# Performance work log

Hardware: AMD Instinct MI355X
Metric: run time of the kernel (lower is better)

## Reference

```python
import jax, jax.numpy as jnp
import numpy as np

C = 128      # hidden_dim
H = 8        # nheads
HD = C // H  # head_dim = 16
SCALE = HD ** (-0.5)
Q = 100      # num_queries
T = 5        # t
DM = 512     # d_model
AD = 128     # audio feature dim
EPS = 1e-5


def _ln(x, g, b):
    m = jnp.mean(x, -1, keepdims=True)
    v = jnp.mean((x - m) ** 2, -1, keepdims=True)
    return (x - m) / jnp.sqrt(v + EPS) * g + b


def _heads(x):
    bt, L, c = x.shape
    return x.reshape(bt, L, H, c // H).transpose(0, 2, 1, 3)  # (bt,H,L,hd)


def _unheads(x):
    bt, h, L, d = x.shape
    return x.transpose(0, 2, 1, 3).reshape(bt, L, h * d)


def _attn(q, k, v):
    a = jax.nn.softmax(jnp.einsum('bhqd,bhkd->bhqk', q, k) * SCALE, axis=-1)
    return jnp.einsum('bhqk,bhkd->bhqd', a, v)


def setup_inputs() -> dict:
    key = jax.random.key(0)
    ks = iter(jax.random.split(key, 40))
    def nrm(shape, s=0.02):
        return jax.random.normal(next(ks), shape, dtype=jnp.float32) * s
    bt, hw = 40, 1024
    return {
        'audio_feat': jax.random.normal(next(ks), (bt, hw, AD), dtype=jnp.float32),
        'vis_feat': jax.random.normal(next(ks), (bt, hw, DM), dtype=jnp.float32),
        'iq_emb': nrm((Q, C), 0.1),
        'w_iqp': nrm((C, 2 * C)), 'b_iqp': jnp.zeros((2 * C,), jnp.float32),
        'w_afp': nrm((AD, 2 * C)), 'b_afp': jnp.zeros((2 * C,), jnp.float32),
        'w_vfp': nrm((DM, 2 * C)), 'b_vfp': jnp.zeros((2 * C,), jnp.float32),
        'g_an': jnp.ones((2 * C,), jnp.float32), 'be_an': jnp.zeros((2 * C,), jnp.float32),
        'g_vn': jnp.ones((2 * C,), jnp.float32), 'be_vn': jnp.zeros((2 * C,), jnp.float32),
        'w_aqp': nrm((C, 2 * C)), 'b_aqp': jnp.zeros((2 * C,), jnp.float32),
        'w_vqp': nrm((C, 2 * C)), 'b_vqp': jnp.zeros((2 * C,), jnp.float32),
        'w_aq': nrm((AD, C)), 'b_aq': jnp.zeros((C,), jnp.float32),
        'w_vq': nrm((DM, C)), 'b_vq': jnp.zeros((C,), jnp.float32),
        'w_in': nrm((C, 3 * C)), 'b_in': jnp.zeros((3 * C,), jnp.float32),
        'w_o': nrm((C, C)), 'b_o': jnp.zeros((C,), jnp.float32),
        'w_ao': nrm((C, DM)), 'b_ao': jnp.zeros((DM,), jnp.float32),
        'w_vo': nrm((C, DM)), 'b_vo': jnp.zeros((DM,), jnp.float32),
    }


def reference(audio_feat, vis_feat, iq_emb, w_iqp, b_iqp, w_afp, b_afp,
              w_vfp, b_vfp, g_an, be_an, g_vn, be_vn, w_aqp, b_aqp,
              w_vqp, b_vqp, w_aq, b_aq, w_vq, b_vq, w_in, b_in, w_o, b_o,
              w_ao, b_ao, w_vo, b_vo):
    bt, hw, _ = vis_feat.shape
    bs = bt // T

    # intermediate query projection -> audio / vis query sets
    aq0, vq0 = jnp.split(iq_emb @ w_iqp + b_iqp, 2, axis=-1)  # (Q, C) each
    aqh = _heads(jnp.broadcast_to(aq0, (bt, Q, C)))
    vqh = _heads(jnp.broadcast_to(vq0, (bt, Q, C)))

    # feature K/V (LayerNorm over 2C then chunk)
    a_ki, a_vi = jnp.split(_ln(audio_feat @ w_afp + b_afp, g_an, be_an), 2, axis=-1)
    v_ki, v_vi = jnp.split(_ln(vis_feat @ w_vfp + b_vfp, g_vn, be_vn), 2, axis=-1)

    # cross-attn: queries attend to features, with residual on queries
    aiq = _unheads(_attn(aqh, _heads(a_ki), _heads(a_vi)) + aqh)  # (bt,Q,C)
    viq = _unheads(_attn(vqh, _heads(v_ki), _heads(v_vi)) + vqh)

    # self-attn over concatenated queries across time (per sample)
    queries = jnp.concatenate([aiq, viq], axis=1).reshape(bs, T * 2 * Q, C)
    qkv = queries @ w_in + b_in
    q, k, v = jnp.split(qkv, 3, axis=-1)
    sa = _unheads(_attn(_heads(q), _heads(k), _heads(v))) @ w_o + b_o
    queries = sa.reshape(bt, 2 * Q, C)
    aiq2, viq2 = queries[:, :Q], queries[:, Q:]

    # fused queries become K/V for the features
    a_kf, a_vf = jnp.split(aiq2 @ w_aqp + b_aqp, 2, axis=-1)
    v_kf, v_vf = jnp.split(viq2 @ w_vqp + b_vqp, 2, axis=-1)
    _a = _heads(audio_feat @ w_aq + b_aq)
    _v = _heads(vis_feat @ w_vq + b_vq)

    a_att = _unheads(_attn(_a, _heads(v_kf), _heads(v_vf)))  # (bt,hw,C)
    audio_out = (a_att + audio_feat) @ w_ao + b_ao            # (bt,hw,DM)

    v_att = _unheads(_attn(_v, _heads(a_kf), _heads(a_vf)))   # (bt,hw,C)
    vis_out = v_att @ w_vo + b_vo + vis_feat                  # (bt,hw,DM)

    return (audio_out, vis_out, aiq2)
```

## Files before the change

### kernel.cpp

```cpp
#include <hip/hip_runtime.h>

#define EPSF 1e-5f
#define SCALEF 0.25f

typedef __attribute__((ext_vector_type(8))) __bf16 bf16x8;
typedef __attribute__((ext_vector_type(8))) unsigned short sh8;
typedef __attribute__((ext_vector_type(4))) float f32x4;

__device__ __forceinline__ unsigned short f2bf(float f) {
  return __builtin_bit_cast(unsigned short, (__bf16)f);
}
__device__ __forceinline__ unsigned pk2(float lo, float hi) {
  return (unsigned)f2bf(lo) | ((unsigned)f2bf(hi) << 16);
}
__device__ __forceinline__ float bf2f(unsigned short u) {
  return __uint_as_float((unsigned)u << 16);
}

__device__ __forceinline__ void gll16(const void* g, void* l) {
  __builtin_amdgcn_global_load_lds((const __attribute__((address_space(1))) void*)g,
                                   (__attribute__((address_space(3))) void*)l,
                                   16, 0, 0);
}

template <int K, int BN, int EPI, bool POST, bool AHEAD, bool OBF, bool PBF, bool QSC>
__global__ __launch_bounds__(BN * 2) void mfma_gemm(
    const unsigned short* __restrict__ A, const unsigned short* __restrict__ Wt,
    const float* __restrict__ bias, const float* __restrict__ post,
    float* __restrict__ C, int M, int Ntot, int ATPB, int CTPB, size_t CPS,
    float* __restrict__ aiq2) {
  constexpr int NW = BN / 32;
  constexpr int NCW = BN / 64;
  __shared__ __align__(16) unsigned short As[128 * 32];
  __shared__ __align__(16) unsigned short Bs[BN * 32];
  const int tid = threadIdx.x;
  const int wid = tid >> 6, lane = tid & 63;
  const int wr = wid / NCW, wc = wid % NCW;
  const int m0t = blockIdx.x * 128, n0t = blockIdx.y * BN;
  const int ir = lane >> 2, sl = lane & 3;
  const int sg = lane >> 4, li = lane & 15;
  f32x4 acc[4][4];
#pragma unroll
  for (int i = 0; i < 4; i++)
#pragma unroll
    for (int j = 0; j < 4; j++) acc[i][j] = (f32x4){0.f, 0.f, 0.f, 0.f};
  constexpr int nIss = 8 + BN / 16;

  for (int k0 = 0; k0 < K; k0 += 32) {
    __syncthreads();
    for (int is = wid; is < nIss; is += NW) {
      if (is < 8) {
        int r = is * 16 + ir;
        int sp = sl ^ ((r >> 1) & 3);
        const unsigned short* gsrc;
        if (AHEAD) {
          int rg = m0t + r;
          if (rg >= M) rg = M - 1;
          int b = rg / ATPB, tok = rg - b * ATPB;
          int e = k0 + sp * 8;
          gsrc = A + ((((size_t)b * 8 + (e >> 4)) * ATPB + tok) << 4) + (e & 15);
        } else {
          gsrc = A + (size_t)(m0t + r) * K + k0 + sp * 8;
        }
        gll16(gsrc, (void*)&As[is * 512]);
      } else {
        int r = (is - 8) * 16 + ir;
        int sp = sl ^ ((r >> 1) & 3);
        gll16(Wt + (size_t)(n0t + r) * K + k0 + sp * 8, (void*)&Bs[(is - 8) * 512]);
      }
    }
    __syncthreads();
    bf16x8 af[4], bfr[4];
#pragma unroll
    for (int mi = 0; mi < 4; mi++) {
      int m = wr * 64 + mi * 16 + li;
      sh8 t = *(const sh8*)&As[m * 32 + ((sg ^ ((m >> 1) & 3)) << 3)];
      af[mi] = __builtin_bit_cast(bf16x8, t);
    }
#pragma unroll
    for (int ni = 0; ni < 4; ni++) {
      int n = wc * 64 + ni * 16 + li;
      sh8 t = *(const sh8*)&Bs[n * 32 + ((sg ^ ((n >> 1) & 3)) << 3)];
      bfr[ni] = __builtin_bit_cast(bf16x8, t);
    }
#pragma unroll
    for (int mi = 0; mi < 4; mi++)
#pragma unroll
      for (int ni = 0; ni < 4; ni++)
        acc[mi][ni] = __builtin_amdgcn_mfma_f32_16x16x32_bf16(af[mi], bfr[ni],
                                                              acc[mi][ni], 0, 0, 0);
  }

  float bv[4];
#pragma unroll
  for (int ni = 0; ni < 4; ni++) bv[ni] = bias[n0t + wc * 64 + ni * 16 + li];

  if constexpr (EPI == 2) {
#pragma unroll
    for (int mi = 0; mi < 4; mi++)
#pragma unroll
      for (int r = 0; r < 4; r++) {
        int mg = m0t + wr * 64 + mi * 16 + sg * 4 + r;
        if (mg < M) {
          int b = mg / CTPB, tok = mg - b * CTPB;
#pragma unroll
          for (int ni = 0; ni < 4; ni++) {
            int col = n0t + wc * 64 + ni * 16 + li;
            float v = acc[mi][ni][r] + bv[ni];
            int pt = col >> 7, h = (col >> 4) & 7, d = col & 15;
            if (QSC && pt == 0) v *= SCALEF;
            size_t idx = ((((size_t)b * 8 + h) * CTPB + tok) << 4) + d;
            if (OBF)
              ((unsigned short*)C + (size_t)pt * CPS)[idx] = f2bf(v);
            else
              (C + (size_t)pt * CPS)[idx] = v;
          }
        }
      }
  } else {
#pragma unroll
    for (int mi = 0; mi < 4; mi++)
#pragma unroll
      for (int r = 0; r < 4; r++) {
        int mrow = m0t + wr * 64 + mi * 16 + sg * 4 + r;
        if (mrow < M) {
#pragma unroll
          for (int ni = 0; ni < 4; ni++) {
            int col = n0t + wc * 64 + ni * 16 + li;
            float v = acc[mi][ni][r] + bv[ni];
            if (POST) {
              if (PBF)
                v += bf2f(((const unsigned short*)post)[(size_t)mrow * Ntot + col]);
              else
                v += post[(size_t)mrow * Ntot + col];
            }
            C[(size_t)mrow * Ntot + col] = v;
            if (aiq2) {
              int fb = mrow / 200, wi2 = mrow % 200;
              if (wi2 < 100) aiq2[((size_t)fb * 100 + wi2) * Ntot + col] = v;
            }
          }
        }
      }
  }
}

__global__ __launch_bounds__(512) void ln_gemm(
    const float* __restrict__ audio, const float* __restrict__ vis,
    const unsigned short* __restrict__ afp_t, const unsigned short* __restrict__ vfp_t,
    const float* __restrict__ b_afp, const float* __restrict__ b_vfp,
    const float* __restrict__ g_an, const float* __restrict__ g_vn,
    const float* __restrict__ be_an, const float* __restrict__ be_vn,
    unsigned short* __restrict__ akn, unsigned short* __restrict__ vkn,
    unsigned short* __restrict__ audio_bf, unsigned short* __restrict__ vis_bf) {
  constexpr int BN = 256, NW = 8, NCW = 4;
  constexpr size_t CPS = 5242880;
  __shared__ __align__(16) unsigned short As[128 * 32];
  __shared__ __align__(16) unsigned short Bs[BN * 32];
  __shared__ float2 part[128][4];
  const int z = blockIdx.z;
  const float* Af32 = z ? vis : audio;
  const unsigned short* Wt = z ? vfp_t : afp_t;
  const float* bias = z ? b_vfp : b_afp;
  const float* gg = z ? g_vn : g_an;
  const float* be = z ? be_vn : be_an;
  unsigned short* C = z ? vkn : akn;
  unsigned short* Aside = z ? vis_bf : audio_bf;
  const int K = z ? 512 : 128;
  const int tid = threadIdx.x;
  const int wid = tid >> 6, lane = tid & 63;
  const int wr = wid / NCW, wc = wid % NCW;
  const int m0t = blockIdx.x * 128;
  const int ir = lane >> 2, sl = lane & 3;
  const int sg = lane >> 4, li = lane & 15;
  f32x4 acc[4][4];
#pragma unroll
  for (int i = 0; i < 4; i++)
#pragma unroll
    for (int j = 0; j < 4; j++) acc[i][j] = (f32x4){0.f, 0.f, 0.f, 0.f};

  for (int k0 = 0; k0 < K; k0 += 32) {
    __syncthreads();
    {
      int r = tid >> 2, slp = tid & 3;
      int sp = slp ^ ((r >> 1) & 3);
      const float4* src = (const float4*)(Af32 + (size_t)(m0t + r) * K + k0 + sp * 8);
      float4 aa = src[0], bb = src[1];
      uint4 w;
      w.x = pk2(aa.x, aa.y); w.y = pk2(aa.z, aa.w);
      w.z = pk2(bb.x, bb.y); w.w = pk2(bb.z, bb.w);
      *(uint4*)&As[r * 32 + slp * 8] = w;
      *(uint4*)(Aside + (size_t)(m0t + r) * K + k0 + sp * 8) = w;
    }
    for (int is = 8 + wid; is < 8 + BN / 16; is += NW) {
      int r2 = (is - 8) * 16 + ir;
      int sp2 = sl ^ ((r2 >> 1) & 3);
      gll16(Wt + (size_t)r2 * K + k0 + sp2 * 8, (void*)&Bs[(is - 8) * 512]);
    }
    __syncthreads();
    bf16x8 af[4], bfr[4];
#pragma unroll
    for (int mi = 0; mi < 4; mi++) {
      int m = wr * 64 + mi * 16 + li;
      sh8 t = *(const sh8*)&As[m * 32 + ((sg ^ ((m >> 1) & 3)) << 3)];
      af[mi] = __builtin_bit_cast(bf16x8, t);
    }
#pragma unroll
    for (int ni = 0; ni < 4; ni++) {
      int n = wc * 64 + ni * 16 + li;
      sh8 t = *(const sh8*)&Bs[n * 32 + ((sg ^ ((n >> 1) & 3)) << 3)];
      bfr[ni] = __builtin_bit_cast(bf16x8, t);
    }
#pragma unroll
    for (int mi = 0; mi < 4; mi++)
#pragma unroll
      for (int ni = 0; ni < 4; ni++)
        acc[mi][ni] = __builtin_amdgcn_mfma_f32_16x16x32_bf16(af[mi], bfr[ni],
                                                              acc[mi][ni], 0, 0, 0);
  }

  float bv[4];
#pragma unroll
  for (int ni = 0; ni < 4; ni++) bv[ni] = bias[wc * 64 + ni * 16 + li];
#pragma unroll
  for (int mi = 0; mi < 4; mi++)
#pragma unroll
    for (int ni = 0; ni < 4; ni++)
#pragma unroll
      for (int r = 0; r < 4; r++) acc[mi][ni][r] += bv[ni];
#pragma unroll
  for (int mi = 0; mi < 4; mi++)
#pragma unroll
    for (int r = 0; r < 4; r++) {
      float s = acc[mi][0][r] + acc[mi][1][r] + acc[mi][2][r] + acc[mi][3][r];
      float q2 = acc[mi][0][r] * acc[mi][0][r] + acc[mi][1][r] * acc[mi][1][r] +
                 acc[mi][2][r] * acc[mi][2][r] + acc[mi][3][r] * acc[mi][3][r];
#pragma unroll
      for (int off = 1; off < 16; off <<= 1) {
        s += __shfl_xor(s, off);
        q2 += __shfl_xor(q2, off);
      }
      if (li == 0) part[wr * 64 + mi * 16 + sg * 4 + r][wc] = make_float2(s, q2);
    }
  __syncthreads();
  float gv[4], bev[4];
#pragma unroll
  for (int ni = 0; ni < 4; ni++) {
    int col = wc * 64 + ni * 16 + li;
    gv[ni] = gg[col];
    bev[ni] = be[col];
  }
#pragma unroll
  for (int mi = 0; mi < 4; mi++)
#pragma unroll
    for (int r = 0; r < 4; r++) {
      int mrow = wr * 64 + mi * 16 + sg * 4 + r;
      float2 p0 = part[mrow][0], p1 = part[mrow][1], p2 = part[mrow][2], p3 = part[mrow][3];
      float S = p0.x + p1.x + p2.x + p3.x;
      float Qq = p0.y + p1.y + p2.y + p3.y;
      float mean = S * (1.f / 256.f);
      float var = Qq * (1.f / 256.f) - mean * mean;
      float rstd = rsqrtf(var + EPSF);
      int mg = m0t + mrow;
      int b = mg >> 10, tok = mg & 1023;
#pragma unroll
      for (int ni = 0; ni < 4; ni++) {
        int col = wc * 64 + ni * 16 + li;
        float val = (acc[mi][ni][r] - mean) * rstd * gv[ni] + bev[ni];
        int half = col >> 7, h = (col >> 4) & 7, d = col & 15;
        size_t idx = ((((size_t)b * 8 + h) * 1024 + tok) << 4) + d;
        (C + (half ? CPS : 0))[idx] = f2bf(val);
      }
    }
}

__global__ __launch_bounds__(256) void projq_kernel(
    const unsigned short* __restrict__ audio_bf, const unsigned short* __restrict__ vis_bf,
    const unsigned short* __restrict__ aq_t, const unsigned short* __restrict__ vq_t,
    const float* __restrict__ b_aq, const float* __restrict__ b_vq,
    unsigned short* __restrict__ a_hm, unsigned short* __restrict__ v_hm) {
  constexpr int BN = 128, NW = 4, NCW = 2;
  __shared__ __align__(16) unsigned short As[128 * 32];
  __shared__ __align__(16) unsigned short Bs[BN * 32];
  const int z = blockIdx.z;
  const unsigned short* A = z ? vis_bf : audio_bf;
  const unsigned short* Wt = z ? vq_t : aq_t;
  const float* bias = z ? b_vq : b_aq;
  unsigned short* C = z ? v_hm : a_hm;
  const int K = z ? 512 : 128;
  const int tid = threadIdx.x;
  const int wid = tid >> 6, lane = tid & 63;
  const int wr = wid / NCW, wc = wid % NCW;
  const int m0t = blockIdx.x * 128;
  const int ir = lane >> 2, sl = lane & 3;
  const int sg = lane >> 4, li = lane & 15;
  f32x4 acc[4][4];
#pragma unroll
  for (int i = 0; i < 4; i++)
#pragma unroll
    for (int j = 0; j < 4; j++) acc[i][j] = (f32x4){0.f, 0.f, 0.f, 0.f};

  for (int k0 = 0; k0 < K; k0 += 32) {
    __syncthreads();
    for (int is = wid; is < 8 + BN / 16; is += NW) {
      if (is < 8) {
        int r = is * 16 + ir;
        int sp = sl ^ ((r >> 1) & 3);
        gll16(A + (size_t)(m0t + r) * K + k0 + sp * 8, (void*)&As[is * 512]);
      } else {
        int r = (is - 8) * 16 + ir;
        int sp = sl ^ ((r >> 1) & 3);
        gll16(Wt + (size_t)r * K + k0 + sp * 8, (void*)&Bs[(is - 8) * 512]);
      }
    }
    __syncthreads();
    bf16x8 af[4], bfr[4];
#pragma unroll
    for (int mi = 0; mi < 4; mi++) {
      int m = wr * 64 + mi * 16 + li;
      sh8 t = *(const sh8*)&As[m * 32 + ((sg ^ ((m >> 1) & 3)) << 3)];
      af[mi] = __builtin_bit_cast(bf16x8, t);
    }
#pragma unroll
    for (int ni = 0; ni < 4; ni++) {
      int n = wc * 64 + ni * 16 + li;
      sh8 t = *(const sh8*)&Bs[n * 32 + ((sg ^ ((n >> 1) & 3)) << 3)];
      bfr[ni] = __builtin_bit_cast(bf16x8, t);
    }
#pragma unroll
    for (int mi = 0; mi < 4; mi++)
#pragma unroll
      for (int ni = 0; ni < 4; ni++)
        acc[mi][ni] = __builtin_amdgcn_mfma_f32_16x16x32_bf16(af[mi], bfr[ni],
                                                              acc[mi][ni], 0, 0, 0);
  }

  float bv[4];
#pragma unroll
  for (int ni = 0; ni < 4; ni++) bv[ni] = bias[wc * 64 + ni * 16 + li];
#pragma unroll
  for (int mi = 0; mi < 4; mi++)
#pragma unroll
    for (int r = 0; r < 4; r++) {
      int mg = m0t + wr * 64 + mi * 16 + sg * 4 + r;
      int b = mg >> 10, tok = mg & 1023;
#pragma unroll
      for (int ni = 0; ni < 4; ni++) {
        int col = wc * 64 + ni * 16 + li;
        float v = (acc[mi][ni][r] + bv[ni]) * SCALEF;
        int h = (col >> 4) & 7, d = col & 15;
        C[((((size_t)b * 8 + h) * 1024 + tok) << 4) + d] = f2bf(v);
      }
    }
}

__global__ __launch_bounds__(512) void mattn1(
    const float* __restrict__ aqvq,
    const unsigned short* __restrict__ akn, const unsigned short* __restrict__ avn,
    const unsigned short* __restrict__ vkn, const unsigned short* __restrict__ vvn,
    unsigned short* __restrict__ op) {
  __shared__ __align__(16) unsigned short Klds[64][24];
  __shared__ __align__(16) unsigned short VTlds[16][72];
  __shared__ __align__(16) unsigned short Plds[8][16][72];
  const int tid = threadIdx.x, wid = tid >> 6, lane = tid & 63;
  const int li = lane & 15, gr = lane >> 4;
  const int z = blockIdx.z, h = blockIdx.y;
  const int mod = z >= 40 ? 1 : 0;
  const int b = z - mod * 40;
  const int bh = b * 8 + h;
  const int qi = wid * 16 + li;
  const bool qact = qi < 100;
  const int qic = qact ? qi : 99;
  const float* qrow = aqvq + mod * 128 + (size_t)qic * 256 + h * 16;
  const unsigned short* kp = mod ? vkn : akn;
  const unsigned short* vp = mod ? vvn : avn;

  sh8 z8 = (sh8)0;
  bf16x8 qf = __builtin_bit_cast(bf16x8, z8);
  if (gr < 2) {
    const float4* q4 = (const float4*)(qrow + gr * 8);
    float4 qa = q4[0], qb = q4[1];
    sh8 tt;
    tt[0] = f2bf(qa.x * SCALEF); tt[1] = f2bf(qa.y * SCALEF);
    tt[2] = f2bf(qa.z * SCALEF); tt[3] = f2bf(qa.w * SCALEF);
    tt[4] = f2bf(qb.x * SCALEF); tt[5] = f2bf(qb.y * SCALEF);
    tt[6] = f2bf(qb.z * SCALEF); tt[7] = f2bf(qb.w * SCALEF);
    qf = __builtin_bit_cast(bf16x8, tt);
  }

  float mrun = -3e38f, lrun = 0.f;
  f32x4 acc = (f32x4){0.f, 0.f, 0.f, 0.f};
  const f32x4 zero4 = (f32x4){0.f, 0.f, 0.f, 0.f};
  const unsigned* Ku = (const unsigned*)(kp + (size_t)bh * 1024 * 16);
  const unsigned* Vu = (const unsigned*)(vp + (size_t)bh * 1024 * 16);
  const int skey = tid >> 3, sdb = tid & 7;

  unsigned kw = Ku[(size_t)skey * 8 + sdb];
  unsigned vw = Vu[(size_t)skey * 8 + sdb];
  for (int kb = 0; kb < 1024; kb += 64) {
    __syncthreads();
    *(unsigned*)&Klds[skey][sdb * 2] = kw;
    VTlds[sdb * 2 + 0][skey] = (unsigned short)(vw & 0xffff);
    VTlds[sdb * 2 + 1][skey] = (unsigned short)(vw >> 16);
    if (kb + 64 < 1024) {
      kw = Ku[(size_t)(kb + 64 + skey) * 8 + sdb];
      vw = Vu[(size_t)(kb + 64 + skey) * 8 + sdb];
    }
    __syncthreads();
    f32x4 st[4];
#pragma unroll
    for (int t = 0; t < 4; t++) {
      sh8 kk = *(const sh8*)&Klds[t * 16 + li][(gr & 1) * 8];
      st[t] = __builtin_amdgcn_mfma_f32_16x16x32_bf16(
          __builtin_bit_cast(bf16x8, kk), qf, zero4, 0, 0, 0);
    }
    float bm = st[0][0];
#pragma unroll
    for (int t = 0; t < 4; t++)
#pragma unroll
      for (int r = 0; r < 4; r++) bm = fmaxf(bm, st[t][r]);
    bm = fmaxf(bm, __shfl_xor(bm, 16));
    bm = fmaxf(bm, __shfl_xor(bm, 32));
    if (bm > mrun + 8.f) {
      float cf = __expf(mrun - bm);
      lrun *= cf;
      acc[0] *= cf; acc[1] *= cf; acc[2] *= cf; acc[3] *= cf;
      mrun = bm;
    }
    float ls = 0.f;
    unsigned pw[4][2];
#pragma unroll
    for (int t = 0; t < 4; t++) {
      float p0 = __expf(st[t][0] - mrun), p1 = __expf(st[t][1] - mrun);
      float p2 = __expf(st[t][2] - mrun), p3 = __expf(st[t][3] - mrun);
      ls += (p0 + p1) + (p2 + p3);
      pw[t][0] = pk2(p0, p1);
      pw[t][1] = pk2(p2, p3);
    }
    ls += __shfl_xor(ls, 16);
    ls += __shfl_xor(ls, 32);
    lrun += ls;
#pragma unroll
    for (int t = 0; t < 4; t++)
      *(uint2*)&Plds[wid][li][t * 16 + gr * 4] = make_uint2(pw[t][0], pw[t][1]);
#pragma unroll
    for (int hh = 0; hh < 2; hh++) {
      sh8 vt = *(const sh8*)&VTlds[li][hh * 32 + gr * 8];
      sh8 pt = *(const sh8*)&Plds[wid][li][hh * 32 + gr * 8];
      acc = __builtin_amdgcn_mfma_f32_16x16x32_bf16(
          __builtin_bit_cast(bf16x8, vt), __builtin_bit_cast(bf16x8, pt), acc, 0, 0, 0);
    }
  }
  float inv = 1.f / lrun;
  float o[4];
#pragma unroll
  for (int r = 0; r < 4; r++) o[r] = acc[r] * inv;
  const float4* q4 = (const float4*)(qrow + gr * 4);
  float4 qv = q4[0];
  o[0] += qv.x; o[1] += qv.y; o[2] += qv.z; o[3] += qv.w;
  if (qact) {
    int obh = (b / 5) * 8 + h;
    int otok = (b % 5) * 200 + mod * 100 + qi;
    *(uint2*)(op + (((size_t)obh * 1000 + otok) << 4) + gr * 4) =
        make_uint2(pk2(o[0], o[1]), pk2(o[2], o[3]));
  }
}

template <int MODE>
__global__ __launch_bounds__(512) void mattn8(
    const unsigned short* __restrict__ q0s, const unsigned short* __restrict__ q1s,
    size_t qsb, size_t qsh, int qsr,
    const unsigned short* __restrict__ k0s, const unsigned short* __restrict__ v0s,
    const unsigned short* __restrict__ k1s, const unsigned short* __restrict__ v1s,
    int nk, int nq, unsigned short* __restrict__ o0s, unsigned short* __restrict__ o1s,
    int OTPB, const unsigned short* __restrict__ residbf) {
  __shared__ __align__(16) unsigned short Klds[64][24];
  __shared__ __align__(16) unsigned short VTlds[16][72];
  __shared__ __align__(16) unsigned short Plds[8][16][72];
  const int tid = threadIdx.x, wid = tid >> 6, lane = tid & 63;
  const int li = lane & 15, gr = lane >> 4;
  const int z = blockIdx.z, h = blockIdx.y;
  int mod = 0, b = z;
  const unsigned short *qp = q0s, *kp = k0s, *vp = v0s;
  unsigned short* op = o0s;
  if (MODE == 2) {
    mod = z >= 40 ? 1 : 0;
    b = z - mod * 40;
    if (mod) { qp = q1s; kp = k1s; vp = v1s; op = o1s; }
  }
  const int bh = b * 8 + h;
  const int qi = blockIdx.x * 128 + wid * 16 + li;
  const bool qact = qi < nq;
  const int qic = qact ? qi : nq - 1;
  const unsigned short* qrow = qp + b * qsb + h * qsh + (size_t)qic * qsr;

  sh8 z8 = (sh8)0;
  bf16x8 qf = __builtin_bit_cast(bf16x8, z8);
  if (gr < 2) qf = __builtin_bit_cast(bf16x8, *(const sh8*)(qrow + gr * 8));

  float mrun = -3e38f, lrun = 0.f;
  f32x4 acc = (f32x4){0.f, 0.f, 0.f, 0.f};
  const f32x4 zero4 = (f32x4){0.f, 0.f, 0.f, 0.f};
  const unsigned* Ku = (const unsigned*)(kp + (size_t)bh * nk * 16);
  const unsigned* Vu = (const unsigned*)(vp + (size_t)bh * nk * 16);
  const int skey = tid >> 3, sdb = tid & 7;

  unsigned kw = (skey < nk) ? Ku[(size_t)skey * 8 + sdb] : 0u;
  unsigned vw = (skey < nk) ? Vu[(size_t)skey * 8 + sdb] : 0u;
  for (int kb = 0; kb < nk; kb += 64) {
    __syncthreads();
    *(unsigned*)&Klds[skey][sdb * 2] = kw;
    VTlds[sdb * 2 + 0][skey] = (unsigned short)(vw & 0xffff);
    VTlds[sdb * 2 + 1][skey] = (unsigned short)(vw >> 16);
    if (kb + 64 < nk) {
      int gk = kb + 64 + skey;
      kw = (gk < nk) ? Ku[(size_t)gk * 8 + sdb] : 0u;
      vw = (gk < nk) ? Vu[(size_t)gk * 8 + sdb] : 0u;
    }
    __syncthreads();
    f32x4 st[4];
#pragma unroll
    for (int t = 0; t < 4; t++) {
      sh8 kk = *(const sh8*)&Klds[t * 16 + li][(gr & 1) * 8];
      st[t] = __builtin_amdgcn_mfma_f32_16x16x32_bf16(
          __builtin_bit_cast(bf16x8, kk), qf, zero4, 0, 0, 0);
    }
    if (kb + 64 > nk) {
#pragma unroll
      for (int t = 0; t < 4; t++) {
        int kbase = kb + t * 16 + gr * 4;
#pragma unroll
        for (int r = 0; r < 4; r++)
          if (kbase + r >= nk) st[t][r] = -1e30f;
      }
    }
    float bm = st[0][0];
#pragma unroll
    for (int t = 0; t < 4; t++)
#pragma unroll
      for (int r = 0; r < 4; r++) bm = fmaxf(bm, st[t][r]);
    bm = fmaxf(bm, __shfl_xor(bm, 16));
    bm = fmaxf(bm, __shfl_xor(bm, 32));
    if (bm > mrun + 8.f) {
      float cf = __expf(mrun - bm);
      lrun *= cf;
      acc[0] *= cf; acc[1] *= cf; acc[2] *= cf; acc[3] *= cf;
      mrun = bm;
    }
    float ls = 0.f;
    unsigned pw[4][2];
#pragma unroll
    for (int t = 0; t < 4; t++) {
      float p0 = __expf(st[t][0] - mrun), p1 = __expf(st[t][1] - mrun);
      float p2 = __expf(st[t][2] - mrun), p3 = __expf(st[t][3] - mrun);
      ls += (p0 + p1) + (p2 + p3);
      pw[t][0] = pk2(p0, p1);
      pw[t][1] = pk2(p2, p3);
    }
    ls += __shfl_xor(ls, 16);
    ls += __shfl_xor(ls, 32);
    lrun += ls;
#pragma unroll
    for (int t = 0; t < 4; t++)
      *(uint2*)&Plds[wid][li][t * 16 + gr * 4] = make_uint2(pw[t][0], pw[t][1]);
#pragma unroll
    for (int hh = 0; hh < 2; hh++) {
      sh8 vt = *(const sh8*)&VTlds[li][hh * 32 + gr * 8];
      sh8 pt = *(const sh8*)&Plds[wid][li][hh * 32 + gr * 8];
      acc = __builtin_amdgcn_mfma_f32_16x16x32_bf16(
          __builtin_bit_cast(bf16x8, vt), __builtin_bit_cast(bf16x8, pt), acc, 0, 0, 0);
    }
  }
  float inv = 1.f / lrun;
  float o[4];
#pragma unroll
  for (int r = 0; r < 4; r++) o[r] = acc[r] * inv;
  if (MODE == 2 && mod == 0 && residbf) {
    uint2 rv = *(const uint2*)(residbf + ((size_t)b * 1024 + qic) * 128 + h * 16 + gr * 4);
    o[0] += bf2f((unsigned short)(rv.x & 0xffff));
    o[1] += bf2f((unsigned short)(rv.x >> 16));
    o[2] += bf2f((unsigned short)(rv.y & 0xffff));
    o[3] += bf2f((unsigned short)(rv.y >> 16));
  }
  if (qact) {
    *(uint2*)(op + (((size_t)bh * OTPB + qi) << 4) + gr * 4) =
        make_uint2(pk2(o[0], o[1]), pk2(o[2], o[3]));
  }
}

__global__ __launch_bounds__(256) void prep_kernel(
    const float* __restrict__ iq, const float* __restrict__ w_iqp,
    const float* __restrict__ b_iqp,
    const float* __restrict__ w_afp, const float* __restrict__ w_vfp,
    const float* __restrict__ w_aq, const float* __restrict__ w_vq,
    const float* __restrict__ w_in, const float* __restrict__ w_o,
    const float* __restrict__ w_ao, const float* __restrict__ w_vo,
    unsigned short* __restrict__ WT, float* __restrict__ aqvq) {
  __shared__ float row[128];
  const int g = blockIdx.x, tid = threadIdx.x;
  if (g < 1728) {
    int lg = g;
    int K, N;
    const float* W;
    unsigned dst;
    if (lg < 128)       { K = 128; N = 256; W = w_afp; dst = 0; }
    else if (lg < 640)  { K = 512; N = 256; W = w_vfp; dst = 32768;  lg -= 128; }
    else if (lg < 704)  { K = 128; N = 128; W = w_aq;  dst = 163840; lg -= 640; }
    else if (lg < 960)  { K = 512; N = 128; W = w_vq;  dst = 180224; lg -= 704; }
    else if (lg < 1152) { K = 128; N = 384; W = w_in;  dst = 245760; lg -= 960; }
    else if (lg < 1216) { K = 128; N = 128; W = w_o;   dst = 294912; lg -= 1152; }
    else if (lg < 1472) { K = 128; N = 512; W = w_ao;  dst = 311296; lg -= 1216; }
    else                { K = 128; N = 512; W = w_vo;  dst = 376832; lg -= 1472; }
    int idx = lg * 256 + tid;
    if (idx < K * N) {
      int k = idx / N, n = idx - k * N;
      WT[dst + (size_t)n * K + k] = f2bf(W[idx]);
    }
  } else {
    int r = g - 1728;
    if (tid < 128) row[tid] = iq[r * 128 + tid];
    __syncthreads();
    float acc = b_iqp[tid];
#pragma unroll 8
    for (int k = 0; k < 128; ++k) acc += row[k] * w_iqp[k * 256 + tid];
    aqvq[r * 256 + tid] = acc;
  }
}

template <int K, int N, int R>
__global__ __launch_bounds__(N) void gemm_kv_kernel(
    const float* __restrict__ in,
    const float* __restrict__ Wa, const float* __restrict__ ba,
    const float* __restrict__ Wv, const float* __restrict__ bvv,
    unsigned short* __restrict__ Ka, unsigned short* __restrict__ Va,
    unsigned short* __restrict__ Kv, unsigned short* __restrict__ Vv) {
  __shared__ float rows[R][K];
  const int sel = blockIdx.y;
  const float* W = sel ? Wv : Wa;
  const float* bias = sel ? bvv : ba;
  unsigned short* outK = sel ? Kv : Ka;
  unsigned short* outV = sel ? Vv : Va;
  const int rowoff = sel ? 100 : 0;
  int r0 = blockIdx.x * R;
  for (int e = threadIdx.x; e < R * K; e += N) {
    int rr = e / K, k = e - rr * K;
    size_t r = r0 + rr;
    size_t irx = (r / 100) * 200 + rowoff + (r % 100);
    rows[rr][k] = in[irx * K + k];
  }
  __syncthreads();
  int c = threadIdx.x;
  float acc[R];
  float bb = bias[c];
#pragma unroll
  for (int rr = 0; rr < R; rr++) acc[rr] = bb;
  for (int k = 0; k < K; k += 4) {
    float w0 = W[(size_t)k * N + c];
    float w1 = W[(size_t)(k + 1) * N + c];
    float w2 = W[(size_t)(k + 2) * N + c];
    float w3 = W[(size_t)(k + 3) * N + c];
#pragma unroll
    for (int rr = 0; rr < R; rr++) {
      float4 r4 = *reinterpret_cast<const float4*>(&rows[rr][k]);
      acc[rr] = fmaf(r4.x, w0, acc[rr]);
      acc[rr] = fmaf(r4.y, w1, acc[rr]);
      acc[rr] = fmaf(r4.z, w2, acc[rr]);
      acc[rr] = fmaf(r4.w, w3, acc[rr]);
    }
  }
  int half = c >> 7, h = (c >> 4) & 7, d = c & 15;
  unsigned short* dst = half ? outV : outK;
#pragma unroll
  for (int rr = 0; rr < R; rr++) {
    int r = r0 + rr;
    int b = r / 100, tok = r - b * 100;
    dst[((((size_t)b * 8 + h) * 100 + tok) << 4) + d] = f2bf(acc[rr]);
  }
}

extern "C" void kernel_launch(void* const* d_in, const int* in_sizes, int n_in,
                              void* d_out, int out_size, void* d_ws, size_t ws_size,
                              hipStream_t stream) {
  const float* audio = (const float*)d_in[0];
  const float* vis   = (const float*)d_in[1];
  const float* iq    = (const float*)d_in[2];
  const float* w_iqp = (const float*)d_in[3];
  const float* b_iqp = (const float*)d_in[4];
  const float* w_afp = (const float*)d_in[5];
  const float* b_afp = (const float*)d_in[6];
  const float* w_vfp = (const float*)d_in[7];
  const float* b_vfp = (const float*)d_in[8];
  const float* g_an  = (const float*)d_in[9];
  const float* be_an = (const float*)d_in[10];
  const float* g_vn  = (const float*)d_in[11];
  const float* be_vn = (const float*)d_in[12];
  const float* w_aqp = (const float*)d_in[13];
  const float* b_aqp = (const float*)d_in[14];
  const float* w_vqp = (const float*)d_in[15];
  const float* b_vqp = (const float*)d_in[16];
  const float* w_aq  = (const float*)d_in[17];
  const float* b_aq  = (const float*)d_in[18];
  const float* w_vq  = (const float*)d_in[19];
  const float* b_vq  = (const float*)d_in[20];
  const float* w_in  = (const float*)d_in[21];
  const float* b_in  = (const float*)d_in[22];
  const float* w_o   = (const float*)d_in[23];
  const float* b_o   = (const float*)d_in[24];
  const float* w_ao  = (const float*)d_in[25];
  const float* b_ao  = (const float*)d_in[26];
  const float* w_vo  = (const float*)d_in[27];
  const float* b_vo  = (const float*)d_in[28];

  float* out = (float*)d_out;
  float* ws  = (float*)d_ws;

  unsigned short* vis_bf = (unsigned short*)(out);
  unsigned short* akn = (unsigned short*)(out + 10485760);
  unsigned short* avn = akn + 5242880;
  unsigned short* vkn = akn + 10485760;
  unsigned short* vvn = akn + 15728640;
  unsigned short* a_hm = (unsigned short*)(out + 20971520);
  unsigned short* v_hm = (unsigned short*)(out + 23592960);
  float* aiq2_out = out + 41943040;
  float* audio_out = out;
  float* vis_out   = out + 20971520;

  unsigned short* WT       = (unsigned short*)(ws);
  unsigned short* audio_bf = (unsigned short*)(ws + 262144);
  unsigned short* Q1hm     = (unsigned short*)(ws + 2883584);
  unsigned short* saphm    = (unsigned short*)(ws + 3395584);
  unsigned short* qkvhm    = (unsigned short*)(ws + 3915776);
  unsigned short* aatthm   = (unsigned short*)(ws + 3915776);
  unsigned short* vatthm   = (unsigned short*)(ws + 6987776);
  float* SA                = ws + 9609216;
  unsigned short* Ka = (unsigned short*)(ws + 10633216);
  unsigned short* Va = Ka + 512000;
  unsigned short* Kv = Ka + 1024000;
  unsigned short* Vv = Ka + 1536000;
  float* aqvq = ws + 12681216;

  unsigned short* afp_t = WT + 0;
  unsigned short* vfp_t = WT + 32768;
  unsigned short* aq_t  = WT + 163840;
  unsigned short* vq_t  = WT + 180224;
  unsigned short* in_t  = WT + 245760;
  unsigned short* o_t   = WT + 294912;
  unsigned short* ao_t  = WT + 311296;
  unsigned short* vo_t  = WT + 376832;

  prep_kernel<<<1828, 256, 0, stream>>>(
      iq, w_iqp, b_iqp, w_afp, w_vfp, w_aq, w_vq, w_in, w_o, w_ao, w_vo, WT, aqvq);

  ln_gemm<<<dim3(320, 1, 2), 512, 0, stream>>>(
      audio, vis, afp_t, vfp_t, b_afp, b_vfp, g_an, g_vn, be_an, be_vn,
      akn, vkn, audio_bf, vis_bf);

  mattn1<<<dim3(1, 8, 80), 512, 0, stream>>>(aqvq, akn, avn, vkn, vvn, Q1hm);

  mfma_gemm<128, 128, 2, false, true, true, false, true><<<dim3(63, 3), 256, 0, stream>>>(
      Q1hm, in_t, b_in, nullptr, (float*)qkvhm, 8000, 384, 1000, 1000, 1024000, nullptr);

  mattn8<1><<<dim3(8, 8, 8), 512, 0, stream>>>(
      qkvhm, nullptr, 128000, 16000, 16, qkvhm + 1024000, qkvhm + 2048000,
      nullptr, nullptr, 1000, 1000, saphm, nullptr, 1000, nullptr);

  mfma_gemm<128, 128, 0, false, true, false, false, false><<<dim3(63, 1), 256, 0, stream>>>(
      saphm, o_t, b_o, nullptr, SA, 8000, 128, 1000, 0, 0, aiq2_out);

  gemm_kv_kernel<128, 256, 16><<<dim3(250, 2), 256, 0, stream>>>(
      SA, w_aqp, b_aqp, w_vqp, b_vqp, Ka, Va, Kv, Vv);

  projq_kernel<<<dim3(320, 1, 2), 256, 0, stream>>>(
      audio_bf, vis_bf, aq_t, vq_t, b_aq, b_vq, a_hm, v_hm);

  mattn8<2><<<dim3(8, 8, 80), 512, 0, stream>>>(
      a_hm, v_hm, 131072, 16384, 16, Kv, Vv, Ka, Va, 100, 1024,
      aatthm, vatthm, 1024, audio_bf);

  mfma_gemm<128, 128, 0, true, true, false, true, false><<<dim3(320, 4), 256, 0, stream>>>(
      vatthm, vo_t, b_vo, (const float*)vis_bf, vis_out, 40960, 512, 1024, 0, 0, nullptr);

  mfma_gemm<128, 128, 0, false, true, false, false, false><<<dim3(320, 4), 256, 0, stream>>>(
      aatthm, ao_t, b_ao, nullptr, audio_out, 40960, 512, 1024, 0, 0, nullptr);
}
```

Baseline: 291.9 us.

## Move KV projection to bf16 MFMA GEMM and merge the two output GEMMs

Replaces the scalar fp32 KV-projection kernel with a bf16 MFMA GEMM that reads a bf16 copy of the self-attention output written directly by the w_o GEMM epilogue. Pre-transposes w_aqp and w_vqp to bf16 in the prep kernel. Merges the vis and audio output projection GEMMs into one launch with a z dimension, reading the fp32 vis residual directly instead of the bf16 copy. This trades extra bf16 rounding in the KV path for fewer launches and tensor-core use, and the vis residual read doubles in bytes.

```diff
diff --git a/kernel.cpp b/kernel.cpp
--- a/kernel.cpp
+++ b/kernel.cpp
@@ -23,10 +23,10 @@
                                    16, 0, 0);
 }
 
-template <int K, int BN, int EPI, bool POST, bool AHEAD, bool OBF, bool PBF, bool QSC>
+template <int K, int BN, int EPI, bool AHEAD, bool OBF, bool QSC, bool CBF>
 __global__ __launch_bounds__(BN * 2) void mfma_gemm(
     const unsigned short* __restrict__ A, const unsigned short* __restrict__ Wt,
-    const float* __restrict__ bias, const float* __restrict__ post,
+    const float* __restrict__ bias,
     float* __restrict__ C, int M, int Ntot, int ATPB, int CTPB, size_t CPS,
     float* __restrict__ aiq2) {
   constexpr int NW = BN / 32;
@@ -128,13 +128,10 @@
           for (int ni = 0; ni < 4; ni++) {
             int col = n0t + wc * 64 + ni * 16 + li;
             float v = acc[mi][ni][r] + bv[ni];
-            if (POST) {
-              if (PBF)
-                v += bf2f(((const unsigned short*)post)[(size_t)mrow * Ntot + col]);
-              else
-                v += post[(size_t)mrow * Ntot + col];
-            }
-            C[(size_t)mrow * Ntot + col] = v;
+            if (CBF)
+              ((unsigned short*)C)[(size_t)mrow * Ntot + col] = f2bf(v);
+            else
+              C[(size_t)mrow * Ntot + col] = v;
             if (aiq2) {
               int fb = mrow / 200, wi2 = mrow % 200;
               if (wi2 < 100) aiq2[((size_t)fb * 100 + wi2) * Ntot + col] = v;
@@ -274,6 +271,94 @@
     }
 }
 
+__global__ __launch_bounds__(512) void kvproj_gemm(
+    const unsigned short* __restrict__ SAb,
+    const unsigned short* __restrict__ aqp_t, const unsigned short* __restrict__ vqp_t,
+    const float* __restrict__ b_aqp, const float* __restrict__ b_vqp,
+    unsigned short* __restrict__ Ka, unsigned short* __restrict__ Va,
+    unsigned short* __restrict__ Kv, unsigned short* __restrict__ Vv) {
+  constexpr int BN = 256, NW = 8, NCW = 4, K = 128;
+  __shared__ __align__(16) unsigned short As[128 * 32];
+  __shared__ __align__(16) unsigned short Bs[BN * 32];
+  const int z = blockIdx.z;
+  const unsigned short* Wt = z ? vqp_t : aqp_t;
+  const float* bias = z ? b_vqp : b_aqp;
+  unsigned short* outK = z ? Kv : Ka;
+  unsigned short* outV = z ? Vv : Va;
+  const int rowoff = z ? 100 : 0;
+  const int tid = threadIdx.x;
+  const int wid = tid >> 6, lane = tid & 63;
+  const int wr = wid / NCW, wc = wid % NCW;
+  const int m0t = blockIdx.x * 128;
+  const int ir = lane >> 2, sl = lane & 3;
+  const int sg = lane >> 4, li = lane & 15;
+  f32x4 acc[4][4];
+#pragma unroll
+  for (int i = 0; i < 4; i++)
+#pragma unroll
+    for (int j = 0; j < 4; j++) acc[i][j] = (f32x4){0.f, 0.f, 0.f, 0.f};
+  constexpr int nIss = 8 + BN / 16;
+
+  for (int k0 = 0; k0 < K; k0 += 32) {
+    __syncthreads();
+    for (int is = wid; is < nIss; is += NW) {
+      if (is < 8) {
+        int r = is * 16 + ir;
+        int rg = m0t + r;
+        if (rg >= 4000) rg = 3999;
+        size_t irx = (size_t)(rg / 100) * 200 + rowoff + (rg % 100);
+        int sp = sl ^ ((r >> 1) & 3);
+        gll16(SAb + irx * 128 + k0 + sp * 8, (void*)&As[is * 512]);
+      } else {
+        int r = (is - 8) * 16 + ir;
+        int sp = sl ^ ((r >> 1) & 3);
+        gll16(Wt + (size_t)r * K + k0 + sp * 8, (void*)&Bs[(is - 8) * 512]);
+      }
+    }
+    __syncthreads();
+    bf16x8 af[4], bfr[4];
+#pragma unroll
+    for (int mi = 0; mi < 4; mi++) {
+      int m = wr * 64 + mi * 16 + li;
+      sh8 t = *(const sh8*)&As[m * 32 + ((sg ^ ((m >> 1) & 3)) << 3)];
+      af[mi] = __builtin_bit_cast(bf16x8, t);
+    }
+#pragma unroll
+    for (int ni = 0; ni < 4; ni++) {
+      int n = wc * 64 + ni * 16 + li;
+      sh8 t = *(const sh8*)&Bs[n * 32 + ((sg ^ ((n >> 1) & 3)) << 3)];
+      bfr[ni] = __builtin_bit_cast(bf16x8, t);
+    }
+#pragma unroll
+    for (int mi = 0; mi < 4; mi++)
+#pragma unroll
+      for (int ni = 0; ni < 4; ni++)
+        acc[mi][ni] = __builtin_amdgcn_mfma_f32_16x16x32_bf16(af[mi], bfr[ni],
+                                                              acc[mi][ni], 0, 0, 0);
+  }
+
+  float bv[4];
+#pragma unroll
+  for (int ni = 0; ni < 4; ni++) bv[ni] = bias[wc * 64 + ni * 16 + li];
+#pragma unroll
+  for (int mi = 0; mi < 4; mi++)
+#pragma unroll
+    for (int r = 0; r < 4; r++) {
+      int mg = m0t + wr * 64 + mi * 16 + sg * 4 + r;
+      if (mg < 4000) {
+        int b = mg / 100, tok = mg - b * 100;
+#pragma unroll
+        for (int ni = 0; ni < 4; ni++) {
+          int col = wc * 64 + ni * 16 + li;
+          float v = acc[mi][ni][r] + bv[ni];
+          int half = col >> 7, h = (col >> 4) & 7, d = col & 15;
+          unsigned short* dst = half ? outV : outK;
+          dst[((((size_t)b * 8 + h) * 100 + tok) << 4) + d] = f2bf(v);
+        }
+      }
+    }
+}
+
 __global__ __launch_bounds__(256) void projq_kernel(
     const unsigned short* __restrict__ audio_bf, const unsigned short* __restrict__ vis_bf,
     const unsigned short* __restrict__ aq_t, const unsigned short* __restrict__ vq_t,
@@ -354,6 +439,88 @@
     }
 }
 
+__global__ __launch_bounds__(256) void out_gemm(
+    const unsigned short* __restrict__ vatthm, const unsigned short* __restrict__ aatthm,
+    const unsigned short* __restrict__ vo_t, const unsigned short* __restrict__ ao_t,
+    const float* __restrict__ b_vo, const float* __restrict__ b_ao,
+    const float* __restrict__ vis, float* __restrict__ vis_out,
+    float* __restrict__ audio_out) {
+  constexpr int BN = 128, NW = 4, NCW = 2, K = 128;
+  __shared__ __align__(16) unsigned short As[128 * 32];
+  __shared__ __align__(16) unsigned short Bs[BN * 32];
+  const int z = blockIdx.z;
+  const unsigned short* A = z ? aatthm : vatthm;
+  const unsigned short* Wt = z ? ao_t : vo_t;
+  const float* bias = z ? b_ao : b_vo;
+  float* C = z ? audio_out : vis_out;
+  const int tid = threadIdx.x;
+  const int wid = tid >> 6, lane = tid & 63;
+  const int wr = wid / NCW, wc = wid % NCW;
+  const int m0t = blockIdx.x * 128, n0t = blockIdx.y * BN;
+  const int ir = lane >> 2, sl = lane & 3;
+  const int sg = lane >> 4, li = lane & 15;
+  f32x4 acc[4][4];
+#pragma unroll
+  for (int i = 0; i < 4; i++)
+#pragma unroll
+    for (int j = 0; j < 4; j++) acc[i][j] = (f32x4){0.f, 0.f, 0.f, 0.f};
+
+  for (int k0 = 0; k0 < K; k0 += 32) {
+    __syncthreads();
+    for (int is = wid; is < 8 + BN / 16; is += NW) {
+      if (is < 8) {
+        int r = is * 16 + ir;
+        int rg = m0t + r;
+        int b = rg >> 10, tok = rg & 1023;
+        int e = k0 + ((sl ^ ((r >> 1) & 3)) << 3);
+        gll16(A + ((((size_t)b * 8 + (e >> 4)) * 1024 + tok) << 4) + (e & 15),
+              (void*)&As[is * 512]);
+      } else {
+        int r = (is - 8) * 16 + ir;
+        int sp = sl ^ ((r >> 1) & 3);
+        gll16(Wt + (size_t)(n0t + r) * K + k0 + sp * 8, (void*)&Bs[(is - 8) * 512]);
+      }
+    }
+    __syncthreads();
+    bf16x8 af[4], bfr[4];
+#pragma unroll
+    for (int mi = 0; mi < 4; mi++) {
+      int m = wr * 64 + mi * 16 + li;
+      sh8 t = *(const sh8*)&As[m * 32 + ((sg ^ ((m >> 1) & 3)) << 3)];
+      af[mi] = __builtin_bit_cast(bf16x8, t);
+    }
+#pragma unroll
+    for (int ni = 0; ni < 4; ni++) {
+      int n = wc * 64 + ni * 16 + li;
+      sh8 t = *(const sh8*)&Bs[n * 32 + ((sg ^ ((n >> 1) & 3)) << 3)];
+      bfr[ni] = __builtin_bit_cast(bf16x8, t);
+    }
+#pragma unroll
+    for (int mi = 0; mi < 4; mi++)
+#pragma unroll
+      for (int ni = 0; ni < 4; ni++)
+        acc[mi][ni] = __builtin_amdgcn_mfma_f32_16x16x32_bf16(af[mi], bfr[ni],
+                                                              acc[mi][ni], 0, 0, 0);
+  }
+
+  float bv[4];
+#pragma unroll
+  for (int ni = 0; ni < 4; ni++) bv[ni] = bias[n0t + wc * 64 + ni * 16 + li];
+#pragma unroll
+  for (int mi = 0; mi < 4; mi++)
+#pragma unroll
+    for (int r = 0; r < 4; r++) {
+      int mrow = m0t + wr * 64 + mi * 16 + sg * 4 + r;
+#pragma unroll
+      for (int ni = 0; ni < 4; ni++) {
+        int col = n0t + wc * 64 + ni * 16 + li;
+        float v = acc[mi][ni][r] + bv[ni];
+        if (z == 0) v += vis[(size_t)mrow * 512 + col];
+        C[(size_t)mrow * 512 + col] = v;
+      }
+    }
+}
+
 __global__ __launch_bounds__(512) void mattn1(
     const float* __restrict__ aqvq,
     const unsigned short* __restrict__ akn, const unsigned short* __restrict__ avn,
@@ -595,10 +762,11 @@
     const float* __restrict__ w_aq, const float* __restrict__ w_vq,
     const float* __restrict__ w_in, const float* __restrict__ w_o,
     const float* __restrict__ w_ao, const float* __restrict__ w_vo,
+    const float* __restrict__ w_aqp, const float* __restrict__ w_vqp,
     unsigned short* __restrict__ WT, float* __restrict__ aqvq) {
   __shared__ float row[128];
   const int g = blockIdx.x, tid = threadIdx.x;
-  if (g < 1728) {
+  if (g < 1984) {
     int lg = g;
     int K, N;
     const float* W;
@@ -610,71 +778,22 @@
     else if (lg < 1152) { K = 128; N = 384; W = w_in;  dst = 245760; lg -= 960; }
     else if (lg < 1216) { K = 128; N = 128; W = w_o;   dst = 294912; lg -= 1152; }
     else if (lg < 1472) { K = 128; N = 512; W = w_ao;  dst = 311296; lg -= 1216; }
-    else                { K = 128; N = 512; W = w_vo;  dst = 376832; lg -= 1472; }
+    else if (lg < 1728) { K = 128; N = 512; W = w_vo;  dst = 376832; lg -= 1472; }
+    else if (lg < 1856) { K = 128; N = 256; W = w_aqp; dst = 442368; lg -= 1728; }
+    else                { K = 128; N = 256; W = w_vqp; dst = 475136; lg -= 1856; }
     int idx = lg * 256 + tid;
     if (idx < K * N) {
       int k = idx / N, n = idx - k * N;
       WT[dst + (size_t)n * K + k] = f2bf(W[idx]);
     }
   } else {
-    int r = g - 1728;
+    int r = g - 1984;
     if (tid < 128) row[tid] = iq[r * 128 + tid];
     __syncthreads();
     float acc = b_iqp[tid];
 #pragma unroll 8
     for (int k = 0; k < 128; ++k) acc += row[k] * w_iqp[k * 256 + tid];
     aqvq[r * 256 + tid] = acc;
-  }
-}
-
-template <int K, int N, int R>
-__global__ __launch_bounds__(N) void gemm_kv_kernel(
-    const float* __restrict__ in,
-    const float* __restrict__ Wa, const float* __restrict__ ba,
-    const float* __restrict__ Wv, const float* __restrict__ bvv,
-    unsigned short* __restrict__ Ka, unsigned short* __restrict__ Va,
-    unsigned short* __restrict__ Kv, unsigned short* __restrict__ Vv) {
-  __shared__ float rows[R][K];
-  const int sel = blockIdx.y;
-  const float* W = sel ? Wv : Wa;
-  const float* bias = sel ? bvv : ba;
-  unsigned short* outK = sel ? Kv : Ka;
-  unsigned short* outV = sel ? Vv : Va;
-  const int rowoff = sel ? 100 : 0;
-  int r0 = blockIdx.x * R;
-  for (int e = threadIdx.x; e < R * K; e += N) {
-    int rr = e / K, k = e - rr * K;
-    size_t r = r0 + rr;
-    size_t irx = (r / 100) * 200 + rowoff + (r % 100);
-    rows[rr][k] = in[irx * K + k];
-  }
-  __syncthreads();
-  int c = threadIdx.x;
-  float acc[R];
-  float bb = bias[c];
-#pragma unroll
-  for (int rr = 0; rr < R; rr++) acc[rr] = bb;
-  for (int k = 0; k < K; k += 4) {
-    float w0 = W[(size_t)k * N + c];
-    float w1 = W[(size_t)(k + 1) * N + c];
-    float w2 = W[(size_t)(k + 2) * N + c];
-    float w3 = W[(size_t)(k + 3) * N + c];
-#pragma unroll
-    for (int rr = 0; rr < R; rr++) {
-      float4 r4 = *reinterpret_cast<const float4*>(&rows[rr][k]);
-      acc[rr] = fmaf(r4.x, w0, acc[rr]);
-      acc[rr] = fmaf(r4.y, w1, acc[rr]);
-      acc[rr] = fmaf(r4.z, w2, acc[rr]);
-      acc[rr] = fmaf(r4.w, w3, acc[rr]);
-    }
-  }
-  int half = c >> 7, h = (c >> 4) & 7, d = c & 15;
-  unsigned short* dst = half ? outV : outK;
-#pragma unroll
-  for (int rr = 0; rr < R; rr++) {
-    int r = r0 + rr;
-    int b = r / 100, tok = r - b * 100;
-    dst[((((size_t)b * 8 + h) * 100 + tok) << 4) + d] = f2bf(acc[rr]);
   }
 }
 
@@ -732,7 +851,7 @@
   unsigned short* qkvhm    = (unsigned short*)(ws + 3915776);
   unsigned short* aatthm   = (unsigned short*)(ws + 3915776);
   unsigned short* vatthm   = (unsigned short*)(ws + 6987776);
-  float* SA                = ws + 9609216;
+  unsigned short* SAb      = (unsigned short*)(ws + 9609216);
   unsigned short* Ka = (unsigned short*)(ws + 10633216);
   unsigned short* Va = Ka + 512000;
   unsigned short* Kv = Ka + 1024000;
@@ -747,9 +866,12 @@
   unsigned short* o_t   = WT + 294912;
   unsigned short* ao_t  = WT + 311296;
   unsigned short* vo_t  = WT + 376832;
-
-  prep_kernel<<<1828, 256, 0, stream>>>(
-      iq, w_iqp, b_iqp, w_afp, w_vfp, w_aq, w_vq, w_in, w_o, w_ao, w_vo, WT, aqvq);
+  unsigned short* aqp_t = WT + 442368;
+  unsigned short* vqp_t = WT + 475136;
+
+  prep_kernel<<<2084, 256, 0, stream>>>(
+      iq, w_iqp, b_iqp, w_afp, w_vfp, w_aq, w_vq, w_in, w_o, w_ao, w_vo,
+      w_aqp, w_vqp, WT, aqvq);
 
   ln_gemm<<<dim3(320, 1, 2), 512, 0, stream>>>(
       audio, vis, afp_t, vfp_t, b_afp, b_vfp, g_an, g_vn, be_an, be_vn,
@@ -757,18 +879,18 @@
 
   mattn1<<<dim3(1, 8, 80), 512, 0, stream>>>(aqvq, akn, avn, vkn, vvn, Q1hm);
 
-  mfma_gemm<128, 128, 2, false, true, true, false, true><<<dim3(63, 3), 256, 0, stream>>>(
-      Q1hm, in_t, b_in, nullptr, (float*)qkvhm, 8000, 384, 1000, 1000, 1024000, nullptr);
+  mfma_gemm<128, 128, 2, true, true, true, false><<<dim3(63, 3), 256, 0, stream>>>(
+      Q1hm, in_t, b_in, (float*)qkvhm, 8000, 384, 1000, 1000, 1024000, nullptr);
 
   mattn8<1><<<dim3(8, 8, 8), 512, 0, stream>>>(
       qkvhm, nullptr, 128000, 16000, 16, qkvhm + 1024000, qkvhm + 2048000,
       nullptr, nullptr, 1000, 1000, saphm, nullptr, 1000, nullptr);
 
-  mfma_gemm<128, 128, 0, false, true, false, false, false><<<dim3(63, 1), 256, 0, stream>>>(
-      saphm, o_t, b_o, nullptr, SA, 8000, 128, 1000, 0, 0, aiq2_out);
-
-  gemm_kv_kernel<128, 256, 16><<<dim3(250, 2), 256, 0, stream>>>(
-      SA, w_aqp, b_aqp, w_vqp, b_vqp, Ka, Va, Kv, Vv);
+  mfma_gemm<128, 128, 0, true, false, false, true><<<dim3(63, 1), 256, 0, stream>>>(
+      saphm, o_t, b_o, (float*)SAb, 8000, 128, 1000, 0, 0, aiq2_out);
+
+  kvproj_gemm<<<dim3(32, 1, 2), 512, 0, stream>>>(
+      SAb, aqp_t, vqp_t, b_aqp, b_vqp, Ka, Va, Kv, Vv);
 
   projq_kernel<<<dim3(320, 1, 2), 256, 0, stream>>>(
       audio_bf, vis_bf, aq_t, vq_t, b_aq, b_vq, a_hm, v_hm);
@@ -777,9 +899,6 @@
       a_hm, v_hm, 131072, 16384, 16, Kv, Vv, Ka, Va, 100, 1024,
       aatthm, vatthm, 1024, audio_bf);
 
-  mfma_gemm<128, 128, 0, true, true, false, true, false><<<dim3(320, 4), 256, 0, stream>>>(
-      vatthm, vo_t, b_vo, (const float*)vis_bf, vis_out, 40960, 512, 1024, 0, 0, nullptr);
-
-  mfma_gemm<128, 128, 0, false, true, false, false, false><<<dim3(320, 4), 256, 0, stream>>>(
-      aatthm, ao_t, b_ao, nullptr, audio_out, 40960, 512, 1024, 0, 0, nullptr);
-}
+  out_gemm<<<dim3(320, 4, 2), 256, 0, stream>>>(
+      vatthm, aatthm, vo_t, ao_t, b_vo, b_ao, vis, vis_out, audio_out);
+}
```

Result: no change. 286.7 us (-1.8%).
